# Performance work log

Measured on AMD Instinct MI355X. Metric: run time of the kernel, lower is better.

## Reference

```python
import jax, jax.numpy as jnp
import numpy as np

IN_CH, D, K = 256, 128, 512

def setup_inputs() -> dict:
    key = jax.random.key(0)
    k1, k2, k3, k4 = jax.random.split(key, 4)
    x = jax.random.normal(k1, (16, IN_CH, 64, 64), dtype=jnp.float32)
    W = jax.random.normal(k2, (D, IN_CH), dtype=jnp.float32) * (1.0 / np.sqrt(IN_CH))
    b = jax.random.normal(k3, (D,), dtype=jnp.float32) * 0.01
    prototypes = jax.random.normal(k4, (K, D), dtype=jnp.float32) * 0.02
    gamma = jnp.asarray(1.0, dtype=jnp.float32)
    return {"x": x, "W": W, "b": b, "prototypes": prototypes, "gamma": gamma}

def reference(x, W, b, prototypes, gamma):
    n, c, h, w = x.shape
    # 1x1 conv projection: [n,c,h,w] -> [n,h,w,d]
    q = jnp.einsum('nchw,dc->nhwd', x, W) + b
    q_flat = q.reshape(n * h * w, -1)                      # [T, d]
    q_norm2 = jnp.sum(q_flat * q_flat, axis=1, keepdims=True)   # [T, 1]
    p_norm2 = jnp.sum(prototypes * prototypes, axis=1)[None, :] # [1, K]
    dist2 = q_norm2 + p_norm2 - 2.0 * (q_flat @ prototypes.T)   # [T, K]
    weights = jax.nn.softmax(-jnp.abs(gamma) * dist2, axis=1)
    return weights.reshape(n, h, w, -1).transpose(0, 3, 1, 2)   # [n, K, h, w]
```

## Files before the change

kernel.cpp:

```cpp
#include <hip/hip_runtime.h>

#define HW 4096
#define NCH 256
#define DIM 128
#define NPROTO 512

typedef __attribute__((ext_vector_type(4))) float f32x4;
typedef __attribute__((ext_vector_type(8))) short s16x8;

__device__ __forceinline__ unsigned short f2bf(float f) {
  union { float f; unsigned u; } v; v.f = f;
  unsigned r = v.u + 0x7fffu + ((v.u >> 16) & 1u);
  return (unsigned short)(r >> 16);
}
__device__ __forceinline__ float bf2f(unsigned short h) {
  union { unsigned u; float f; } v; v.u = ((unsigned)h) << 16;
  return v.f;
}

__global__ __launch_bounds__(256) void prep_kernel(const float* __restrict__ P,
                                                   unsigned short* __restrict__ Pr,
                                                   float* __restrict__ pn2) {
  const int tid = threadIdx.x;
  const int n  = blockIdx.x * 64 + (tid >> 2);
  const int qt = tid & 3;
  const float* row = P + n * DIM + qt * 32;
  unsigned short* dst = Pr + ((size_t)qt * NPROTO + n) * 32;
  float ssq = 0.f;
#pragma unroll
  for (int u = 0; u < 8; ++u) {
    f32x4 v = *(const f32x4*)(row + 4 * u);
    ssq += v.x * v.x + v.y * v.y + v.z * v.z + v.w * v.w;
    dst[4 * u + 0] = f2bf(v.x);
    dst[4 * u + 1] = f2bf(v.y);
    dst[4 * u + 2] = f2bf(v.z);
    dst[4 * u + 3] = f2bf(v.w);
  }
  ssq += __shfl_xor(ssq, 1);
  ssq += __shfl_xor(ssq, 2);
  if (qt == 0) pn2[n] = ssq;
}

__global__ __launch_bounds__(512) void proj_kernel(const float* __restrict__ x,
                                                   const float* __restrict__ Wm,
                                                   const float* __restrict__ bias,
                                                   unsigned short* __restrict__ qbf) {
  __shared__ __align__(16) unsigned short x_s[128 * 72];
  __shared__ __align__(16) unsigned short w_s[128 * 72];
  const int tid  = threadIdx.x;
  const int p0   = blockIdx.x * 128;
  const int nimg = p0 >> 12;
  const int hw0  = p0 & 4095;
  const float* xbase = x + (size_t)nimg * NCH * HW + hw0;
  const int wave = tid >> 6, lane = tid & 63;
  const int l15 = lane & 15, l4 = lane >> 4;

  f32x4 acc[8];
#pragma unroll
  for (int j = 0; j < 8; ++j)
#pragma unroll
    for (int r = 0; r < 4; ++r) acc[j][r] = 0.f;

  for (int c0 = 0; c0 < NCH; c0 += 64) {
    {
      const int f = tid & 31, cl = tid >> 5;
#pragma unroll
      for (int r = 0; r < 4; ++r) {
        const int cc = cl + 16 * r;
        f32x4 v = *(const f32x4*)(xbase + (size_t)(c0 + cc) * HW + 4 * f);
        x_s[(4 * f + 0) * 72 + cc] = f2bf(v.x);
        x_s[(4 * f + 1) * 72 + cc] = f2bf(v.y);
        x_s[(4 * f + 2) * 72 + cc] = f2bf(v.z);
        x_s[(4 * f + 3) * 72 + cc] = f2bf(v.w);
      }
      const int f2 = tid & 15, dl = tid >> 4;
#pragma unroll
      for (int r = 0; r < 4; ++r) {
        const int d = dl + 32 * r;
        f32x4 v = *(const f32x4*)(Wm + d * NCH + c0 + 4 * f2);
        unsigned short* w = &w_s[d * 72 + 4 * f2];
        w[0] = f2bf(v.x); w[1] = f2bf(v.y); w[2] = f2bf(v.z); w[3] = f2bf(v.w);
      }
    }
    __syncthreads();
#pragma unroll
    for (int kc = 0; kc < 64; kc += 32) {
      s16x8 a = *(const s16x8*)&x_s[(16 * wave + l15) * 72 + kc + 8 * l4];
#pragma unroll
      for (int j = 0; j < 8; ++j) {
        s16x8 b = *(const s16x8*)&w_s[(16 * j + l15) * 72 + kc + 8 * l4];
        acc[j] = __builtin_amdgcn_mfma_f32_16x16x32_bf16(a, b, acc[j], 0, 0, 0);
      }
    }
    __syncthreads();
  }
  const int mb = 16 * wave + 4 * l4;
#pragma unroll
  for (int j = 0; j < 8; ++j) {
    const int d = 16 * j + l15;
    const float bv = bias[d];
#pragma unroll
    for (int r = 0; r < 4; ++r)
      qbf[(size_t)(p0 + mb + r) * DIM + d] = f2bf(acc[j][r] + bv);
  }
}

__global__ __launch_bounds__(512) void attn_kernel(const unsigned short* __restrict__ qbf,
                                                   const unsigned short* __restrict__ Pr,
                                                   const float* __restrict__ pn2,
                                                   const float* __restrict__ gptr,
                                                   float* __restrict__ out) {
  __shared__ __align__(16) char smem[58368];
  unsigned short* q_s = (unsigned short*)smem;
  unsigned short* P_s = (unsigned short*)(smem + 17408);
  unsigned short* w_s = (unsigned short*)smem;
  float* red  = (float*)(smem + 36864);
  float* rmx  = (float*)(smem + 36864 + 2048);
  float* rinv = (float*)(smem + 36864 + 2048 + 256);

  const int tid  = threadIdx.x;
  const int p0   = blockIdx.x * 64;
  const int nimg = p0 >> 12;
  const int hw0  = p0 & 4095;
  const int wave = tid >> 6, lane = tid & 63;
  const int l15 = lane & 15, l4 = lane >> 4;
  const float g = fabsf(gptr[0]);

  {
    const int r = tid >> 3, c8 = tid & 7;
#pragma unroll
    for (int it = 0; it < 2; ++it) {
      const int col = c8 + 8 * it;
      s16x8 v = *(const s16x8*)(qbf + (size_t)(p0 + r) * DIM + 8 * col);
      *(s16x8*)&q_s[r * 136 + 8 * col] = v;
    }
  }

  f32x4 acc[4][4];
#pragma unroll
  for (int i = 0; i < 4; ++i)
#pragma unroll
    for (int j = 0; j < 4; ++j)
#pragma unroll
      for (int r = 0; r < 4; ++r) acc[i][j][r] = 0.f;

  for (int ch = 0; ch < 4; ++ch) {
    if (ch) __syncthreads();
    {
      const unsigned short* src = Pr + ((size_t)ch * NPROTO + tid) * 32;
      unsigned short* dst = &P_s[tid * 40];
#pragma unroll
      for (int u = 0; u < 4; ++u)
        *(s16x8*)(dst + 8 * u) = *(const s16x8*)(src + 8 * u);
    }
    __syncthreads();
    const int dk = ch * 32;
    s16x8 afr[4];
#pragma unroll
    for (int i = 0; i < 4; ++i)
      afr[i] = *(const s16x8*)&q_s[(16 * i + l15) * 136 + dk + 8 * l4];
#pragma unroll
    for (int j = 0; j < 4; ++j) {
      s16x8 bfr = *(const s16x8*)&P_s[(64 * wave + 16 * j + l15) * 40 + 8 * l4];
#pragma unroll
      for (int i = 0; i < 4; ++i)
        acc[i][j] = __builtin_amdgcn_mfma_f32_16x16x32_bf16(afr[i], bfr, acc[i][j], 0, 0, 0);
    }
  }
  __syncthreads();

  float pnv[4];
#pragma unroll
  for (int j = 0; j < 4; ++j) pnv[j] = pn2[64 * wave + 16 * j + l15];

#pragma unroll
  for (int i = 0; i < 4; ++i)
#pragma unroll
    for (int r = 0; r < 4; ++r) {
      float m = -1e30f;
#pragma unroll
      for (int j = 0; j < 4; ++j) {
        float lv = g * (2.f * acc[i][j][r] - pnv[j]);
        acc[i][j][r] = lv;
        m = fmaxf(m, lv);
      }
#pragma unroll
      for (int s = 1; s < 16; s <<= 1) m = fmaxf(m, __shfl_xor(m, s));
      if (l15 == 0) red[wave * 64 + 16 * i + 4 * l4 + r] = m;
    }
  __syncthreads();
  if (tid < 64) {
    float M = red[tid];
#pragma unroll
    for (int w = 1; w < 8; ++w) M = fmaxf(M, red[w * 64 + tid]);
    rmx[tid] = M;
  }
  __syncthreads();

#pragma unroll
  for (int i = 0; i < 4; ++i)
#pragma unroll
    for (int r = 0; r < 4; ++r) {
      const float M = rmx[16 * i + 4 * l4 + r];
      float s = 0.f;
#pragma unroll
      for (int j = 0; j < 4; ++j) {
        float e = __expf(acc[i][j][r] - M);
        acc[i][j][r] = e;
        s += e;
      }
#pragma unroll
      for (int t = 1; t < 16; t <<= 1) s += __shfl_xor(s, t);
      if (l15 == 0) red[wave * 64 + 16 * i + 4 * l4 + r] = s;
    }
  __syncthreads();
  if (tid < 64) {
    float S = 0.f;
#pragma unroll
    for (int w = 0; w < 8; ++w) S += red[w * 64 + tid];
    rinv[tid] = 1.f / S;
  }
  __syncthreads();

  float inv[4][4];
#pragma unroll
  for (int i = 0; i < 4; ++i)
#pragma unroll
    for (int r = 0; r < 4; ++r) inv[i][r] = rinv[16 * i + 4 * l4 + r];

  const size_t outbase = (size_t)nimg * NPROTO * HW + hw0;
#pragma unroll
  for (int half = 0; half < 2; ++half) {
    if ((wave >> 2) == half) {
      const int wl = wave & 3;
#pragma unroll
      for (int i = 0; i < 4; ++i)
#pragma unroll
        for (int j = 0; j < 4; ++j) {
          const int nl = 64 * wl + 16 * j + l15;
#pragma unroll
          for (int r = 0; r < 4; ++r)
            w_s[nl * 72 + 16 * i + 4 * l4 + r] = f2bf(acc[i][j][r] * inv[i][r]);
        }
    }
    __syncthreads();
    {
      const int f4 = tid & 15, kl = tid >> 4;
#pragma unroll
      for (int it = 0; it < 8; ++it) {
        const int kloc = kl + 32 * it;
        const unsigned short* src = &w_s[kloc * 72 + 4 * f4];
        f32x4 o;
        o.x = bf2f(src[0]); o.y = bf2f(src[1]);
        o.z = bf2f(src[2]); o.w = bf2f(src[3]);
        *(f32x4*)(out + outbase + (size_t)(half * 256 + kloc) * HW + 4 * f4) = o;
      }
    }
    __syncthreads();
  }
}

extern "C" void kernel_launch(void* const* d_in, const int* in_sizes, int n_in,
                              void* d_out, int out_size, void* d_ws, size_t ws_size,
                              hipStream_t stream) {
  const float* x     = (const float*)d_in[0];
  const float* Wm    = (const float*)d_in[1];
  const float* bias  = (const float*)d_in[2];
  const float* prot  = (const float*)d_in[3];
  const float* gamma = (const float*)d_in[4];
  float* out = (float*)d_out;

  unsigned short* q_ws  = (unsigned short*)d_ws;
  unsigned short* P_ws  = (unsigned short*)((char*)d_ws + 16777216);
  float*          pn2_w = (float*)((char*)d_ws + 16777216 + 131072);

  prep_kernel<<<8, 256, 0, stream>>>(prot, P_ws, pn2_w);
  proj_kernel<<<512, 512, 0, stream>>>(x, Wm, bias, q_ws);
  attn_kernel<<<1024, 512, 0, stream>>>(q_ws, P_ws, pn2_w, gamma, out);
}
```

Baseline: 224.8 us.

## Pre-convert W to bf16, async-load it into LDS, register-only attention epilogue

The prep kernel now also converts W to bf16, and the projection kernel streams the bf16 W tiles into a swizzled LDS layout with global_load_lds instead of converting them per block. The attention kernel is restructured into 256-thread blocks over 32 pixels. Each wave reads its q and prototype fragments directly from global memory without LDS staging, and the softmax uses exp2 with a prescaled gamma. Output is written straight from MFMA registers as fp32 vectors, with no LDS transpose and no bf16 round-trip. The aim is to cut LDS traffic and syncs, at the cost of more redundant global reads of q and prototypes and narrower 16-byte strided output stores.

```diff
diff --git a/kernel.cpp b/kernel.cpp
--- a/kernel.cpp
+++ b/kernel.cpp
@@ -13,40 +13,55 @@
   unsigned r = v.u + 0x7fffu + ((v.u >> 16) & 1u);
   return (unsigned short)(r >> 16);
 }
-__device__ __forceinline__ float bf2f(unsigned short h) {
-  union { unsigned u; float f; } v; v.u = ((unsigned)h) << 16;
-  return v.f;
+
+__device__ __forceinline__ void gload_lds16(const void* g, void* l) {
+  __builtin_amdgcn_global_load_lds(
+      (const __attribute__((address_space(1))) void*)g,
+      (__attribute__((address_space(3))) void*)l, 16, 0, 0);
 }
 
 __global__ __launch_bounds__(256) void prep_kernel(const float* __restrict__ P,
-                                                   unsigned short* __restrict__ Pr,
+                                                   const float* __restrict__ Wm,
+                                                   unsigned short* __restrict__ Pbf,
+                                                   unsigned short* __restrict__ Wbf,
                                                    float* __restrict__ pn2) {
   const int tid = threadIdx.x;
-  const int n  = blockIdx.x * 64 + (tid >> 2);
-  const int qt = tid & 3;
-  const float* row = P + n * DIM + qt * 32;
-  unsigned short* dst = Pr + ((size_t)qt * NPROTO + n) * 32;
-  float ssq = 0.f;
-#pragma unroll
-  for (int u = 0; u < 8; ++u) {
-    f32x4 v = *(const f32x4*)(row + 4 * u);
-    ssq += v.x * v.x + v.y * v.y + v.z * v.z + v.w * v.w;
-    dst[4 * u + 0] = f2bf(v.x);
-    dst[4 * u + 1] = f2bf(v.y);
-    dst[4 * u + 2] = f2bf(v.z);
-    dst[4 * u + 3] = f2bf(v.w);
-  }
-  ssq += __shfl_xor(ssq, 1);
-  ssq += __shfl_xor(ssq, 2);
-  if (qt == 0) pn2[n] = ssq;
+  const int b = blockIdx.x;
+  if (b < 8) {
+    const int n  = b * 64 + (tid >> 2);
+    const int qt = tid & 3;
+    const float* row = P + n * DIM + qt * 32;
+    unsigned short* dst = Pbf + (size_t)n * DIM + qt * 32;
+    float ssq = 0.f;
+#pragma unroll
+    for (int u = 0; u < 8; ++u) {
+      f32x4 v = *(const f32x4*)(row + 4 * u);
+      ssq += v.x * v.x + v.y * v.y + v.z * v.z + v.w * v.w;
+      dst[4 * u + 0] = f2bf(v.x);
+      dst[4 * u + 1] = f2bf(v.y);
+      dst[4 * u + 2] = f2bf(v.z);
+      dst[4 * u + 3] = f2bf(v.w);
+    }
+    ssq += __shfl_xor(ssq, 1);
+    ssq += __shfl_xor(ssq, 2);
+    if (qt == 0) pn2[n] = ssq;
+  } else {
+    const int idx = ((b - 8) * 256 + tid) * 16;
+#pragma unroll
+    for (int u = 0; u < 4; ++u) {
+      f32x4 v = *(const f32x4*)(Wm + idx + 4 * u);
+      unsigned short* d = Wbf + idx + 4 * u;
+      d[0] = f2bf(v.x); d[1] = f2bf(v.y); d[2] = f2bf(v.z); d[3] = f2bf(v.w);
+    }
+  }
 }
 
 __global__ __launch_bounds__(512) void proj_kernel(const float* __restrict__ x,
-                                                   const float* __restrict__ Wm,
+                                                   const unsigned short* __restrict__ Wbf,
                                                    const float* __restrict__ bias,
                                                    unsigned short* __restrict__ qbf) {
   __shared__ __align__(16) unsigned short x_s[128 * 72];
-  __shared__ __align__(16) unsigned short w_s[128 * 72];
+  __shared__ __align__(16) unsigned short w_s[128 * 64];
   const int tid  = threadIdx.x;
   const int p0   = blockIdx.x * 128;
   const int nimg = p0 >> 12;
@@ -61,7 +76,17 @@
 #pragma unroll
     for (int r = 0; r < 4; ++r) acc[j][r] = 0.f;
 
+  const int wrow0 = 8 * wave + (lane >> 3);
+  const int wc8   = lane & 7;
+
   for (int c0 = 0; c0 < NCH; c0 += 64) {
+#pragma unroll
+    for (int t = 0; t < 2; ++t) {
+      const int row = 64 * t + wrow0;
+      const unsigned short* src =
+          Wbf + (size_t)row * NCH + c0 + ((wc8 ^ (row & 7)) << 3);
+      gload_lds16(src, (char*)w_s + t * 8192 + wave * 1024);
+    }
     {
       const int f = tid & 31, cl = tid >> 5;
 #pragma unroll
@@ -73,22 +98,15 @@
         x_s[(4 * f + 2) * 72 + cc] = f2bf(v.z);
         x_s[(4 * f + 3) * 72 + cc] = f2bf(v.w);
       }
-      const int f2 = tid & 15, dl = tid >> 4;
-#pragma unroll
-      for (int r = 0; r < 4; ++r) {
-        const int d = dl + 32 * r;
-        f32x4 v = *(const f32x4*)(Wm + d * NCH + c0 + 4 * f2);
-        unsigned short* w = &w_s[d * 72 + 4 * f2];
-        w[0] = f2bf(v.x); w[1] = f2bf(v.y); w[2] = f2bf(v.z); w[3] = f2bf(v.w);
-      }
     }
     __syncthreads();
 #pragma unroll
     for (int kc = 0; kc < 64; kc += 32) {
       s16x8 a = *(const s16x8*)&x_s[(16 * wave + l15) * 72 + kc + 8 * l4];
+      const int ub = (kc >> 3) + l4;
 #pragma unroll
       for (int j = 0; j < 8; ++j) {
-        s16x8 b = *(const s16x8*)&w_s[(16 * j + l15) * 72 + kc + 8 * l4];
+        s16x8 b = *(const s16x8*)&w_s[(16 * j + l15) * 64 + ((ub ^ (l15 & 7)) << 3)];
         acc[j] = __builtin_amdgcn_mfma_f32_16x16x32_bf16(a, b, acc[j], 0, 0, 0);
       }
     }
@@ -105,158 +123,122 @@
   }
 }
 
-__global__ __launch_bounds__(512) void attn_kernel(const unsigned short* __restrict__ qbf,
-                                                   const unsigned short* __restrict__ Pr,
-                                                   const float* __restrict__ pn2,
-                                                   const float* __restrict__ gptr,
-                                                   float* __restrict__ out) {
-  __shared__ __align__(16) char smem[58368];
-  unsigned short* q_s = (unsigned short*)smem;
-  unsigned short* P_s = (unsigned short*)(smem + 17408);
-  unsigned short* w_s = (unsigned short*)smem;
-  float* red  = (float*)(smem + 36864);
-  float* rmx  = (float*)(smem + 36864 + 2048);
-  float* rinv = (float*)(smem + 36864 + 2048 + 256);
+__global__ __launch_bounds__(256, 4) void attn_kernel(const unsigned short* __restrict__ qbf,
+                                                      const unsigned short* __restrict__ Pbf,
+                                                      const float* __restrict__ pn2,
+                                                      const float* __restrict__ gptr,
+                                                      float* __restrict__ out) {
+  __shared__ float red[4 * 32];
+  __shared__ float rmx[32];
+  __shared__ float rinv[32];
 
   const int tid  = threadIdx.x;
-  const int p0   = blockIdx.x * 64;
+  const int p0   = blockIdx.x * 32;
   const int nimg = p0 >> 12;
   const int hw0  = p0 & 4095;
-  const int wave = tid >> 6, lane = tid & 63;
+  const int wv = tid >> 6, lane = tid & 63;
   const int l15 = lane & 15, l4 = lane >> 4;
-  const float g = fabsf(gptr[0]);
-
-  {
-    const int r = tid >> 3, c8 = tid & 7;
-#pragma unroll
-    for (int it = 0; it < 2; ++it) {
-      const int col = c8 + 8 * it;
-      s16x8 v = *(const s16x8*)(qbf + (size_t)(p0 + r) * DIM + 8 * col);
-      *(s16x8*)&q_s[r * 136 + 8 * col] = v;
-    }
-  }
-
-  f32x4 acc[4][4];
-#pragma unroll
-  for (int i = 0; i < 4; ++i)
-#pragma unroll
-    for (int j = 0; j < 4; ++j)
+
+  const float g2  = fabsf(gptr[0]) * 1.44269504088896340736f;
+  const float tg2 = 2.f * g2;
+
+  f32x4 acc[2][8];
+#pragma unroll
+  for (int i = 0; i < 2; ++i)
+#pragma unroll
+    for (int j = 0; j < 8; ++j)
 #pragma unroll
       for (int r = 0; r < 4; ++r) acc[i][j][r] = 0.f;
 
+  const unsigned short* qrow = qbf + (size_t)(p0 + l15) * DIM + 8 * l4;
+  const unsigned short* prow = Pbf + (size_t)(128 * wv + l15) * DIM + 8 * l4;
+
+#pragma unroll
   for (int ch = 0; ch < 4; ++ch) {
-    if (ch) __syncthreads();
-    {
-      const unsigned short* src = Pr + ((size_t)ch * NPROTO + tid) * 32;
-      unsigned short* dst = &P_s[tid * 40];
-#pragma unroll
-      for (int u = 0; u < 4; ++u)
-        *(s16x8*)(dst + 8 * u) = *(const s16x8*)(src + 8 * u);
-    }
-    __syncthreads();
-    const int dk = ch * 32;
-    s16x8 afr[4];
-#pragma unroll
-    for (int i = 0; i < 4; ++i)
-      afr[i] = *(const s16x8*)&q_s[(16 * i + l15) * 136 + dk + 8 * l4];
-#pragma unroll
-    for (int j = 0; j < 4; ++j) {
-      s16x8 bfr = *(const s16x8*)&P_s[(64 * wave + 16 * j + l15) * 40 + 8 * l4];
-#pragma unroll
-      for (int i = 0; i < 4; ++i)
+    const int dk = 32 * ch;
+    s16x8 afr[2];
+#pragma unroll
+    for (int i = 0; i < 2; ++i)
+      afr[i] = *(const s16x8*)(qrow + (size_t)(16 * i) * DIM + dk);
+#pragma unroll
+    for (int j = 0; j < 8; ++j) {
+      s16x8 bfr = *(const s16x8*)(prow + (size_t)(16 * j) * DIM + dk);
+#pragma unroll
+      for (int i = 0; i < 2; ++i)
         acc[i][j] = __builtin_amdgcn_mfma_f32_16x16x32_bf16(afr[i], bfr, acc[i][j], 0, 0, 0);
     }
   }
-  __syncthreads();
-
-  float pnv[4];
-#pragma unroll
-  for (int j = 0; j < 4; ++j) pnv[j] = pn2[64 * wave + 16 * j + l15];
-
-#pragma unroll
-  for (int i = 0; i < 4; ++i)
+
+  float cj[8];
+#pragma unroll
+  for (int j = 0; j < 8; ++j) cj[j] = g2 * pn2[128 * wv + 16 * j + l15];
+
+  const int rbase = 4 * l4;
+
+#pragma unroll
+  for (int i = 0; i < 2; ++i)
 #pragma unroll
     for (int r = 0; r < 4; ++r) {
       float m = -1e30f;
 #pragma unroll
-      for (int j = 0; j < 4; ++j) {
-        float lv = g * (2.f * acc[i][j][r] - pnv[j]);
+      for (int j = 0; j < 8; ++j) {
+        float lv = fmaf(acc[i][j][r], tg2, -cj[j]);
         acc[i][j][r] = lv;
         m = fmaxf(m, lv);
       }
 #pragma unroll
       for (int s = 1; s < 16; s <<= 1) m = fmaxf(m, __shfl_xor(m, s));
-      if (l15 == 0) red[wave * 64 + 16 * i + 4 * l4 + r] = m;
-    }
-  __syncthreads();
-  if (tid < 64) {
+      if (l15 == 0) red[wv * 32 + 16 * i + rbase + r] = m;
+    }
+  __syncthreads();
+  if (tid < 32) {
     float M = red[tid];
 #pragma unroll
-    for (int w = 1; w < 8; ++w) M = fmaxf(M, red[w * 64 + tid]);
+    for (int w = 1; w < 4; ++w) M = fmaxf(M, red[w * 32 + tid]);
     rmx[tid] = M;
   }
   __syncthreads();
 
 #pragma unroll
-  for (int i = 0; i < 4; ++i)
+  for (int i = 0; i < 2; ++i)
 #pragma unroll
     for (int r = 0; r < 4; ++r) {
-      const float M = rmx[16 * i + 4 * l4 + r];
+      const float M = rmx[16 * i + rbase + r];
       float s = 0.f;
 #pragma unroll
-      for (int j = 0; j < 4; ++j) {
-        float e = __expf(acc[i][j][r] - M);
+      for (int j = 0; j < 8; ++j) {
+        float e = exp2f(acc[i][j][r] - M);
         acc[i][j][r] = e;
         s += e;
       }
 #pragma unroll
       for (int t = 1; t < 16; t <<= 1) s += __shfl_xor(s, t);
-      if (l15 == 0) red[wave * 64 + 16 * i + 4 * l4 + r] = s;
-    }
-  __syncthreads();
-  if (tid < 64) {
-    float S = 0.f;
-#pragma unroll
-    for (int w = 0; w < 8; ++w) S += red[w * 64 + tid];
+      if (l15 == 0) red[wv * 32 + 16 * i + rbase + r] = s;
+    }
+  __syncthreads();
+  if (tid < 32) {
+    float S = red[tid] + red[32 + tid] + red[64 + tid] + red[96 + tid];
     rinv[tid] = 1.f / S;
   }
   __syncthreads();
 
-  float inv[4][4];
-#pragma unroll
-  for (int i = 0; i < 4; ++i)
-#pragma unroll
-    for (int r = 0; r < 4; ++r) inv[i][r] = rinv[16 * i + 4 * l4 + r];
-
-  const size_t outbase = (size_t)nimg * NPROTO * HW + hw0;
-#pragma unroll
-  for (int half = 0; half < 2; ++half) {
-    if ((wave >> 2) == half) {
-      const int wl = wave & 3;
-#pragma unroll
-      for (int i = 0; i < 4; ++i)
-#pragma unroll
-        for (int j = 0; j < 4; ++j) {
-          const int nl = 64 * wl + 16 * j + l15;
-#pragma unroll
-          for (int r = 0; r < 4; ++r)
-            w_s[nl * 72 + 16 * i + 4 * l4 + r] = f2bf(acc[i][j][r] * inv[i][r]);
-        }
-    }
-    __syncthreads();
-    {
-      const int f4 = tid & 15, kl = tid >> 4;
-#pragma unroll
-      for (int it = 0; it < 8; ++it) {
-        const int kloc = kl + 32 * it;
-        const unsigned short* src = &w_s[kloc * 72 + 4 * f4];
-        f32x4 o;
-        o.x = bf2f(src[0]); o.y = bf2f(src[1]);
-        o.z = bf2f(src[2]); o.w = bf2f(src[3]);
-        *(f32x4*)(out + outbase + (size_t)(half * 256 + kloc) * HW + 4 * f4) = o;
-      }
-    }
-    __syncthreads();
+  float inv[2][4];
+#pragma unroll
+  for (int i = 0; i < 2; ++i)
+#pragma unroll
+    for (int r = 0; r < 4; ++r) inv[i][r] = rinv[16 * i + rbase + r];
+
+  float* obase = out + (size_t)nimg * NPROTO * HW + hw0;
+#pragma unroll
+  for (int i = 0; i < 2; ++i) {
+    const int px = 16 * i + rbase;
+#pragma unroll
+    for (int j = 0; j < 8; ++j) {
+      const int k = 128 * wv + 16 * j + l15;
+      f32x4 o = acc[i][j];
+      o.x *= inv[i][0]; o.y *= inv[i][1]; o.z *= inv[i][2]; o.w *= inv[i][3];
+      *(f32x4*)(obase + (size_t)k * HW + px) = o;
+    }
   }
 }
 
@@ -273,8 +255,9 @@
   unsigned short* q_ws  = (unsigned short*)d_ws;
   unsigned short* P_ws  = (unsigned short*)((char*)d_ws + 16777216);
   float*          pn2_w = (float*)((char*)d_ws + 16777216 + 131072);
-
-  prep_kernel<<<8, 256, 0, stream>>>(prot, P_ws, pn2_w);
-  proj_kernel<<<512, 512, 0, stream>>>(x, Wm, bias, q_ws);
-  attn_kernel<<<1024, 512, 0, stream>>>(q_ws, P_ws, pn2_w, gamma, out);
-}
+  unsigned short* W_ws  = (unsigned short*)((char*)d_ws + 16777216 + 131072 + 2048);
+
+  prep_kernel<<<16, 256, 0, stream>>>(prot, Wm, P_ws, W_ws, pn2_w);
+  proj_kernel<<<512, 512, 0, stream>>>(x, W_ws, bias, q_ws);
+  attn_kernel<<<2048, 256, 0, stream>>>(q_ws, P_ws, pn2_w, gamma, out);
+}
```

Result: slower. 250.9 us (+11.6%).

## Fuse projection into softmax kernel and write output directly from registers

Applied to the files above, without the earlier changes.

Merges the 1x1-conv projection into the attention kernel, so each block computes its own 64-pixel q tile in shared memory and the bf16 q round trip through global memory goes away. W is pre-converted to bf16 in the prep kernel and loaded with global_load_lds into an XOR-swizzled layout. Prototype chunks are prefetched into registers one step ahead. The softmax uses exp2 with gamma folded into the log2 scale. The output is stored straight from MFMA registers as f32 vectors instead of being staged through LDS as bf16, which also stops rounding the output to bf16. In exchange, the projection work per block is halved in width (64 pixels instead of 128), and the direct stores are less coalesced (4 floats per lane, strided by HW).

```diff
diff --git a/kernel.cpp b/kernel.cpp
--- a/kernel.cpp
+++ b/kernel.cpp
@@ -13,110 +13,62 @@
   unsigned r = v.u + 0x7fffu + ((v.u >> 16) & 1u);
   return (unsigned short)(r >> 16);
 }
-__device__ __forceinline__ float bf2f(unsigned short h) {
-  union { unsigned u; float f; } v; v.u = ((unsigned)h) << 16;
-  return v.f;
+
+__device__ __forceinline__ void gload_lds16(const void* g, void* l) {
+  __builtin_amdgcn_global_load_lds(
+      (const __attribute__((address_space(1))) void*)g,
+      (__attribute__((address_space(3))) void*)l, 16, 0, 0);
 }
 
 __global__ __launch_bounds__(256) void prep_kernel(const float* __restrict__ P,
+                                                   const float* __restrict__ Wm,
                                                    unsigned short* __restrict__ Pr,
+                                                   unsigned short* __restrict__ Wbf,
                                                    float* __restrict__ pn2) {
   const int tid = threadIdx.x;
-  const int n  = blockIdx.x * 64 + (tid >> 2);
-  const int qt = tid & 3;
-  const float* row = P + n * DIM + qt * 32;
-  unsigned short* dst = Pr + ((size_t)qt * NPROTO + n) * 32;
-  float ssq = 0.f;
-#pragma unroll
-  for (int u = 0; u < 8; ++u) {
-    f32x4 v = *(const f32x4*)(row + 4 * u);
-    ssq += v.x * v.x + v.y * v.y + v.z * v.z + v.w * v.w;
-    dst[4 * u + 0] = f2bf(v.x);
-    dst[4 * u + 1] = f2bf(v.y);
-    dst[4 * u + 2] = f2bf(v.z);
-    dst[4 * u + 3] = f2bf(v.w);
-  }
-  ssq += __shfl_xor(ssq, 1);
-  ssq += __shfl_xor(ssq, 2);
-  if (qt == 0) pn2[n] = ssq;
-}
-
-__global__ __launch_bounds__(512) void proj_kernel(const float* __restrict__ x,
-                                                   const float* __restrict__ Wm,
-                                                   const float* __restrict__ bias,
-                                                   unsigned short* __restrict__ qbf) {
-  __shared__ __align__(16) unsigned short x_s[128 * 72];
-  __shared__ __align__(16) unsigned short w_s[128 * 72];
-  const int tid  = threadIdx.x;
-  const int p0   = blockIdx.x * 128;
-  const int nimg = p0 >> 12;
-  const int hw0  = p0 & 4095;
-  const float* xbase = x + (size_t)nimg * NCH * HW + hw0;
-  const int wave = tid >> 6, lane = tid & 63;
-  const int l15 = lane & 15, l4 = lane >> 4;
-
-  f32x4 acc[8];
-#pragma unroll
-  for (int j = 0; j < 8; ++j)
-#pragma unroll
-    for (int r = 0; r < 4; ++r) acc[j][r] = 0.f;
-
-  for (int c0 = 0; c0 < NCH; c0 += 64) {
-    {
-      const int f = tid & 31, cl = tid >> 5;
-#pragma unroll
-      for (int r = 0; r < 4; ++r) {
-        const int cc = cl + 16 * r;
-        f32x4 v = *(const f32x4*)(xbase + (size_t)(c0 + cc) * HW + 4 * f);
-        x_s[(4 * f + 0) * 72 + cc] = f2bf(v.x);
-        x_s[(4 * f + 1) * 72 + cc] = f2bf(v.y);
-        x_s[(4 * f + 2) * 72 + cc] = f2bf(v.z);
-        x_s[(4 * f + 3) * 72 + cc] = f2bf(v.w);
-      }
-      const int f2 = tid & 15, dl = tid >> 4;
-#pragma unroll
-      for (int r = 0; r < 4; ++r) {
-        const int d = dl + 32 * r;
-        f32x4 v = *(const f32x4*)(Wm + d * NCH + c0 + 4 * f2);
-        unsigned short* w = &w_s[d * 72 + 4 * f2];
-        w[0] = f2bf(v.x); w[1] = f2bf(v.y); w[2] = f2bf(v.z); w[3] = f2bf(v.w);
-      }
-    }
-    __syncthreads();
-#pragma unroll
-    for (int kc = 0; kc < 64; kc += 32) {
-      s16x8 a = *(const s16x8*)&x_s[(16 * wave + l15) * 72 + kc + 8 * l4];
-#pragma unroll
-      for (int j = 0; j < 8; ++j) {
-        s16x8 b = *(const s16x8*)&w_s[(16 * j + l15) * 72 + kc + 8 * l4];
-        acc[j] = __builtin_amdgcn_mfma_f32_16x16x32_bf16(a, b, acc[j], 0, 0, 0);
-      }
-    }
-    __syncthreads();
-  }
-  const int mb = 16 * wave + 4 * l4;
-#pragma unroll
-  for (int j = 0; j < 8; ++j) {
-    const int d = 16 * j + l15;
-    const float bv = bias[d];
-#pragma unroll
-    for (int r = 0; r < 4; ++r)
-      qbf[(size_t)(p0 + mb + r) * DIM + d] = f2bf(acc[j][r] + bv);
-  }
-}
-
-__global__ __launch_bounds__(512) void attn_kernel(const unsigned short* __restrict__ qbf,
-                                                   const unsigned short* __restrict__ Pr,
-                                                   const float* __restrict__ pn2,
-                                                   const float* __restrict__ gptr,
-                                                   float* __restrict__ out) {
-  __shared__ __align__(16) char smem[58368];
+  const int b = blockIdx.x;
+  if (b < 8) {
+    const int n  = b * 64 + (tid >> 2);
+    const int qt = tid & 3;
+    const float* row = P + n * DIM + qt * 32;
+    unsigned short* dst = Pr + ((size_t)qt * NPROTO + n) * 32;
+    float ssq = 0.f;
+#pragma unroll
+    for (int u = 0; u < 8; ++u) {
+      f32x4 v = *(const f32x4*)(row + 4 * u);
+      ssq += v.x * v.x + v.y * v.y + v.z * v.z + v.w * v.w;
+      dst[4 * u + 0] = f2bf(v.x);
+      dst[4 * u + 1] = f2bf(v.y);
+      dst[4 * u + 2] = f2bf(v.z);
+      dst[4 * u + 3] = f2bf(v.w);
+    }
+    ssq += __shfl_xor(ssq, 1);
+    ssq += __shfl_xor(ssq, 2);
+    if (qt == 0) pn2[n] = ssq;
+  } else {
+    const int idx = ((b - 8) * 256 + tid) * 16;
+#pragma unroll
+    for (int u = 0; u < 4; ++u) {
+      f32x4 v = *(const f32x4*)(Wm + idx + 4 * u);
+      unsigned short* d = Wbf + idx + 4 * u;
+      d[0] = f2bf(v.x); d[1] = f2bf(v.y); d[2] = f2bf(v.z); d[3] = f2bf(v.w);
+    }
+  }
+}
+
+__global__ __launch_bounds__(512, 4) void fused_kernel(
+    const float* __restrict__ x, const unsigned short* __restrict__ Wbf,
+    const float* __restrict__ bias, const unsigned short* __restrict__ Pr,
+    const float* __restrict__ pn2, const float* __restrict__ gptr,
+    float* __restrict__ out) {
+  __shared__ __align__(16) char smem[61440];
   unsigned short* q_s = (unsigned short*)smem;
+  char*           x_b = smem + 17408;
+  unsigned short* w_s = (unsigned short*)(smem + 17408 + 9216);
   unsigned short* P_s = (unsigned short*)(smem + 17408);
-  unsigned short* w_s = (unsigned short*)smem;
-  float* red  = (float*)(smem + 36864);
-  float* rmx  = (float*)(smem + 36864 + 2048);
-  float* rinv = (float*)(smem + 36864 + 2048 + 256);
+  float* red  = (float*)(smem + 58880);
+  float* rmx  = (float*)(smem + 60928);
+  float* rinv = (float*)(smem + 61184);
 
   const int tid  = threadIdx.x;
   const int p0   = blockIdx.x * 64;
@@ -124,16 +76,78 @@
   const int hw0  = p0 & 4095;
   const int wave = tid >> 6, lane = tid & 63;
   const int l15 = lane & 15, l4 = lane >> 4;
-  const float g = fabsf(gptr[0]);
-
+  const int wr = wave >> 2, wc = wave & 3;
+
+  f32x4 acc1[2][2];
+#pragma unroll
+  for (int i = 0; i < 2; ++i)
+#pragma unroll
+    for (int j = 0; j < 2; ++j)
+#pragma unroll
+      for (int r = 0; r < 4; ++r) acc1[i][j][r] = 0.f;
+
+  const float* xb = x + (size_t)nimg * NCH * HW + hw0;
+  const int f  = tid & 15;
+  const int cp = tid >> 4;
+  const int wrow = 8 * wave + (lane >> 3);
+  const int wu   = lane & 7;
+
+  for (int c0 = 0; c0 < NCH; c0 += 64) {
+#pragma unroll
+    for (int t = 0; t < 2; ++t) {
+      const int row = 64 * t + wrow;
+      const unsigned short* src =
+          Wbf + (size_t)row * NCH + c0 + ((wu ^ (row & 7)) << 3);
+      gload_lds16(src, (char*)w_s + t * 8192 + wave * 1024);
+    }
+    f32x4 v0 = *(const f32x4*)(xb + (size_t)(c0 + 2 * cp + 0) * HW + 4 * f);
+    f32x4 v1 = *(const f32x4*)(xb + (size_t)(c0 + 2 * cp + 1) * HW + 4 * f);
+#pragma unroll
+    for (int s = 0; s < 4; ++s) {
+      const int row = 4 * f + s;
+      unsigned pk = (unsigned)f2bf(v0[s]) | ((unsigned)f2bf(v1[s]) << 16);
+      *(unsigned*)(x_b + row * 144 + ((4 * cp) ^ (((row >> 2) & 7) << 4))) = pk;
+    }
+    __syncthreads();
+#pragma unroll
+    for (int kc = 0; kc < 64; kc += 32) {
+      const int ub = (kc >> 3) + l4;
+      s16x8 a[2];
+#pragma unroll
+      for (int i = 0; i < 2; ++i) {
+        const int row = 32 * wr + 16 * i + l15;
+        a[i] = *(const s16x8*)(x_b + row * 144 + 16 * (ub ^ ((row >> 2) & 7)));
+      }
+#pragma unroll
+      for (int j = 0; j < 2; ++j) {
+        s16x8 b = *(const s16x8*)&w_s[(32 * wc + 16 * j + l15) * 64 +
+                                      ((ub ^ (l15 & 7)) << 3)];
+#pragma unroll
+        for (int i = 0; i < 2; ++i)
+          acc1[i][j] = __builtin_amdgcn_mfma_f32_16x16x32_bf16(a[i], b, acc1[i][j], 0, 0, 0);
+      }
+    }
+    __syncthreads();
+  }
+
+#pragma unroll
+  for (int j = 0; j < 2; ++j) {
+    const int d = 32 * wc + 16 * j + l15;
+    const float bv = bias[d];
+#pragma unroll
+    for (int i = 0; i < 2; ++i) {
+      const int px = 32 * wr + 16 * i + 4 * l4;
+#pragma unroll
+      for (int r = 0; r < 4; ++r)
+        q_s[(px + r) * 136 + d] = f2bf(acc1[i][j][r] + bv);
+    }
+  }
+
+  s16x8 pf[4];
   {
-    const int r = tid >> 3, c8 = tid & 7;
-#pragma unroll
-    for (int it = 0; it < 2; ++it) {
-      const int col = c8 + 8 * it;
-      s16x8 v = *(const s16x8*)(qbf + (size_t)(p0 + r) * DIM + 8 * col);
-      *(s16x8*)&q_s[r * 136 + 8 * col] = v;
-    }
+    const unsigned short* ps = Pr + (size_t)tid * 32;
+#pragma unroll
+    for (int u = 0; u < 4; ++u) pf[u] = *(const s16x8*)(ps + 8 * u);
   }
 
   f32x4 acc[4][4];
@@ -145,16 +159,19 @@
       for (int r = 0; r < 4; ++r) acc[i][j][r] = 0.f;
 
   for (int ch = 0; ch < 4; ++ch) {
-    if (ch) __syncthreads();
+    __syncthreads();
     {
-      const unsigned short* src = Pr + ((size_t)ch * NPROTO + tid) * 32;
       unsigned short* dst = &P_s[tid * 40];
 #pragma unroll
-      for (int u = 0; u < 4; ++u)
-        *(s16x8*)(dst + 8 * u) = *(const s16x8*)(src + 8 * u);
-    }
-    __syncthreads();
-    const int dk = ch * 32;
+      for (int u = 0; u < 4; ++u) *(s16x8*)(dst + 8 * u) = pf[u];
+    }
+    __syncthreads();
+    if (ch < 3) {
+      const unsigned short* ps = Pr + (size_t)((ch + 1) * NPROTO + tid) * 32;
+#pragma unroll
+      for (int u = 0; u < 4; ++u) pf[u] = *(const s16x8*)(ps + 8 * u);
+    }
+    const int dk = 32 * ch;
     s16x8 afr[4];
 #pragma unroll
     for (int i = 0; i < 4; ++i)
@@ -167,11 +184,12 @@
         acc[i][j] = __builtin_amdgcn_mfma_f32_16x16x32_bf16(afr[i], bfr, acc[i][j], 0, 0, 0);
     }
   }
-  __syncthreads();
-
-  float pnv[4];
-#pragma unroll
-  for (int j = 0; j < 4; ++j) pnv[j] = pn2[64 * wave + 16 * j + l15];
+
+  const float g2  = fabsf(gptr[0]) * 1.44269504088896340736f;
+  const float tg2 = 2.f * g2;
+  float cj[4];
+#pragma unroll
+  for (int j = 0; j < 4; ++j) cj[j] = g2 * pn2[64 * wave + 16 * j + l15];
 
 #pragma unroll
   for (int i = 0; i < 4; ++i)
@@ -180,7 +198,7 @@
       float m = -1e30f;
 #pragma unroll
       for (int j = 0; j < 4; ++j) {
-        float lv = g * (2.f * acc[i][j][r] - pnv[j]);
+        float lv = fmaf(acc[i][j][r], tg2, -cj[j]);
         acc[i][j][r] = lv;
         m = fmaxf(m, lv);
       }
@@ -198,14 +216,14 @@
   __syncthreads();
 
 #pragma unroll
-  for (int i = 0; i < 4; ++i)
+  for (int i = 0; i < 4; ++i) {
+    const f32x4 Mi = *(const f32x4*)&rmx[16 * i + 4 * l4];
 #pragma unroll
     for (int r = 0; r < 4; ++r) {
-      const float M = rmx[16 * i + 4 * l4 + r];
       float s = 0.f;
 #pragma unroll
       for (int j = 0; j < 4; ++j) {
-        float e = __expf(acc[i][j][r] - M);
+        float e = exp2f(acc[i][j][r] - Mi[r]);
         acc[i][j][r] = e;
         s += e;
       }
@@ -213,6 +231,7 @@
       for (int t = 1; t < 16; t <<= 1) s += __shfl_xor(s, t);
       if (l15 == 0) red[wave * 64 + 16 * i + 4 * l4 + r] = s;
     }
+  }
   __syncthreads();
   if (tid < 64) {
     float S = 0.f;
@@ -222,41 +241,17 @@
   }
   __syncthreads();
 
-  float inv[4][4];
-#pragma unroll
-  for (int i = 0; i < 4; ++i)
-#pragma unroll
-    for (int r = 0; r < 4; ++r) inv[i][r] = rinv[16 * i + 4 * l4 + r];
-
-  const size_t outbase = (size_t)nimg * NPROTO * HW + hw0;
-#pragma unroll
-  for (int half = 0; half < 2; ++half) {
-    if ((wave >> 2) == half) {
-      const int wl = wave & 3;
-#pragma unroll
-      for (int i = 0; i < 4; ++i)
-#pragma unroll
-        for (int j = 0; j < 4; ++j) {
-          const int nl = 64 * wl + 16 * j + l15;
-#pragma unroll
-          for (int r = 0; r < 4; ++r)
-            w_s[nl * 72 + 16 * i + 4 * l4 + r] = f2bf(acc[i][j][r] * inv[i][r]);
-        }
-    }
-    __syncthreads();
-    {
-      const int f4 = tid & 15, kl = tid >> 4;
-#pragma unroll
-      for (int it = 0; it < 8; ++it) {
-        const int kloc = kl + 32 * it;
-        const unsigned short* src = &w_s[kloc * 72 + 4 * f4];
-        f32x4 o;
-        o.x = bf2f(src[0]); o.y = bf2f(src[1]);
-        o.z = bf2f(src[2]); o.w = bf2f(src[3]);
-        *(f32x4*)(out + outbase + (size_t)(half * 256 + kloc) * HW + 4 * f4) = o;
-      }
-    }
-    __syncthreads();
+  float* ob = out + (size_t)nimg * NPROTO * HW + hw0;
+#pragma unroll
+  for (int i = 0; i < 4; ++i) {
+    const f32x4 iv = *(const f32x4*)&rinv[16 * i + 4 * l4];
+    const int px = 16 * i + 4 * l4;
+#pragma unroll
+    for (int j = 0; j < 4; ++j) {
+      const int k = 64 * wave + 16 * j + l15;
+      f32x4 o = acc[i][j] * iv;
+      *(f32x4*)(ob + (size_t)k * HW + px) = o;
+    }
   }
 }
 
@@ -270,11 +265,10 @@
   const float* gamma = (const float*)d_in[4];
   float* out = (float*)d_out;
 
-  unsigned short* q_ws  = (unsigned short*)d_ws;
-  unsigned short* P_ws  = (unsigned short*)((char*)d_ws + 16777216);
-  float*          pn2_w = (float*)((char*)d_ws + 16777216 + 131072);
-
-  prep_kernel<<<8, 256, 0, stream>>>(prot, P_ws, pn2_w);
-  proj_kernel<<<512, 512, 0, stream>>>(x, Wm, bias, q_ws);
-  attn_kernel<<<1024, 512, 0, stream>>>(q_ws, P_ws, pn2_w, gamma, out);
-}
+  unsigned short* Pr_w  = (unsigned short*)d_ws;
+  float*          pn2_w = (float*)((char*)d_ws + 131072);
+  unsigned short* W_ws  = (unsigned short*)((char*)d_ws + 131072 + 2048);
+
+  prep_kernel<<<16, 256, 0, stream>>>(prot, Wm, Pr_w, W_ws, pn2_w);
+  fused_kernel<<<1024, 512, 0, stream>>>(x, W_ws, bias, Pr_w, pn2_w, gamma, out);
+}
```

After: 215.5 us. 4.2% less time.
